# Kernel optimization log

Hardware: AMD Instinct MI355X
Metric: run time of the kernel (lower is better)

The kernel has to match this reference:

```python
import jax, jax.numpy as jnp
import numpy as np
import math

B, S, D, H, L, DFF = 64, 512, 512, 8, 2, 1024
DK = D // H
NEG = -1e32
LN_EPS = 1e-5


def cosine_pos_emb(seqlen, d_model):
    # pe[:,0::2]=sin(pos*div), pe[:,1::2]=cos(pos*div) -- fully overwrites the randn init
    pos = jnp.arange(seqlen, dtype=jnp.float32)[:, None]
    div = jnp.exp(jnp.arange(0, d_model, 2, dtype=jnp.float32) * (-math.log(10000.0) / d_model))
    ang = pos * div  # [S, D/2]
    return jnp.stack([jnp.sin(ang), jnp.cos(ang)], axis=-1).reshape(seqlen, d_model)


def layernorm(x, g, b):
    m = jnp.mean(x, axis=-1, keepdims=True)
    v = jnp.var(x, axis=-1, keepdims=True)
    return g * (x - m) * jax.lax.rsqrt(v + LN_EPS) + b


def setup_inputs() -> dict:
    key = jax.random.key(0)
    ks = jax.random.split(key, 8)
    sc = 0.02
    inp = {
        'q_embed_data': jax.random.normal(ks[0], (B, S, D), jnp.float32),
        'qa_embed_data': jax.random.normal(ks[1], (B, S, D), jnp.float32),
        'forget_rate': jax.random.uniform(ks[2], (B, 1, S, 1), jnp.float32),
        # per-block params, leading dim = n_blocks (kq_same=1: q uses k_linear)
        'Wk': jax.random.normal(ks[3], (L, D, D), jnp.float32) * sc,
        'bk': jnp.zeros((L, D), jnp.float32),
        'Wv': jax.random.normal(ks[4], (L, D, D), jnp.float32) * sc,
        'bv': jnp.zeros((L, D), jnp.float32),
        'Wo': jax.random.normal(ks[5], (L, D, D), jnp.float32) * sc,
        'bo': jnp.zeros((L, D), jnp.float32),
        'ln1_g': jnp.ones((L, D), jnp.float32),
        'ln1_b': jnp.zeros((L, D), jnp.float32),
        'W1': jax.random.normal(ks[6], (L, D, DFF), jnp.float32) * sc,
        'b1': jnp.zeros((L, DFF), jnp.float32),
        'W2': jax.random.normal(ks[7], (L, DFF, D), jnp.float32) * sc,
        'b2': jnp.zeros((L, D), jnp.float32),
        'ln2_g': jnp.ones((L, D), jnp.float32),
        'ln2_b': jnp.zeros((L, D), jnp.float32),
    }
    return inp


def reference(q_embed_data, qa_embed_data, forget_rate, Wk, bk, Wv, bv, Wo, bo,
              ln1_g, ln1_b, W1, b1, W2, b2, ln2_g, ln2_b):
    pe = cosine_pos_emb(S, D)
    x = q_embed_data + pe  # query/key stream
    y = qa_embed_data + pe  # value stream (fixed across blocks)
    # mask=0 path: np.triu(ones, k=0) == 0 -> strictly lower-triangular allowed
    allow = jnp.tril(jnp.ones((S, S), dtype=bool), -1)
    scale = 1.0 / math.sqrt(DK)
    for i in range(L):
        qk = (x @ Wk[i] + bk[i]).reshape(B, S, H, DK).transpose(0, 2, 1, 3)  # [B,H,S,dk]
        v = (y @ Wv[i] + bv[i]).reshape(B, S, H, DK).transpose(0, 2, 1, 3)
        scores = jnp.einsum('bhqd,bhkd->bhqk', qk, qk) * scale
        scores = scores * forget_rate  # [B,1,S,1] broadcasts over heads and keys
        scores = jnp.where(allow, scores, NEG)
        p = jax.nn.softmax(scores, axis=-1)
        p = p.at[:, :, 0, :].set(0.0)  # zero_pad: first query row zeroed
        attn = jnp.einsum('bhqk,bhkd->bhqd', p, v).transpose(0, 2, 1, 3).reshape(B, S, D)
        attn = attn @ Wo[i] + bo[i]
        x = layernorm(x + attn, ln1_g[i], ln1_b[i])
        ff = jax.nn.relu(x @ W1[i] + b1[i]) @ W2[i] + b2[i]
        x = layernorm(x + ff, ln2_g[i], ln2_b[i])
    return x
```

## Files before the change

### kernel.cpp

```cpp
#include <hip/hip_runtime.h>
#include <cstdio>

#define B_   64
#define S_   512
#define D_   512
#define H_   8
#define DK_  64
#define DFF_ 1024
#define L_   2
#define BS_  (B_ * S_)

typedef __attribute__((ext_vector_type(8))) short bf16x8;
typedef __attribute__((ext_vector_type(4))) short bf16x4;
typedef __attribute__((ext_vector_type(4))) float f32x4;

__device__ inline short f2bf(float f) {
  unsigned u = __float_as_uint(f);
  u = u + 0x7FFF + ((u >> 16) & 1);
  return (short)(u >> 16);
}
__device__ inline float bf2f(short s) {
  return __uint_as_float(((unsigned)(unsigned short)s) << 16);
}

__device__ inline void gl_lds16(const short* g, void* lds_base) {
  __builtin_amdgcn_global_load_lds(
      (const __attribute__((address_space(1))) void*)g,
      (__attribute__((address_space(3))) void*)lds_base, 16, 0, 0);
}

__global__ void pe_kernel(float* __restrict__ pe) {
  int idx = blockIdx.x * 256 + threadIdx.x;
  int s = idx >> 9, d = idx & 511;
  float dv = __expf((float)(d & ~1) * (-9.210340371976184f / (float)D_));
  float ang = (float)s * dv;
  pe[idx] = (d & 1) ? cosf(ang) : sinf(ang);
}

__global__ __launch_bounds__(256) void prep_kernel(
    const float* __restrict__ q, const float* __restrict__ qa,
    const float* __restrict__ pe,
    short* __restrict__ xb, short* __restrict__ yb) {
  size_t base = ((size_t)blockIdx.x * 256 + threadIdx.x) * 8;
  int sd = (int)(base & (size_t)(S_ * D_ - 1));
  f32x4 p0 = *(const f32x4*)(pe + sd);
  f32x4 p1 = *(const f32x4*)(pe + sd + 4);
  f32x4 q0 = *(const f32x4*)(q + base);
  f32x4 q1 = *(const f32x4*)(q + base + 4);
  f32x4 a0 = *(const f32x4*)(qa + base);
  f32x4 a1 = *(const f32x4*)(qa + base + 4);
  bf16x8 xv, yv;
#pragma unroll
  for (int i = 0; i < 4; ++i) {
    xv[i] = f2bf(q0[i] + p0[i]);
    yv[i] = f2bf(a0[i] + p0[i]);
  }
#pragma unroll
  for (int i = 0; i < 4; ++i) {
    xv[4 + i] = f2bf(q1[i] + p1[i]);
    yv[4 + i] = f2bf(a1[i] + p1[i]);
  }
  *(bf16x8*)(xb + base) = xv;
  *(bf16x8*)(yb + base) = yv;
}

struct TrArgs {
  const float* src[10];
  short* dst[10];
  int R[10], C[10];
};
__global__ __launch_bounds__(256) void tr_w_all(TrArgs a) {
  const int slot = blockIdx.z;
  const int R = a.R[slot], C = a.C[slot];
  const int c0 = blockIdx.x * 64, r0 = blockIdx.y * 64;
  if (c0 >= C || r0 >= R) return;
  const float* __restrict__ src = a.src[slot];
  short* __restrict__ dst = a.dst[slot];
  __shared__ short Ts[64][72];
  const int t = threadIdx.x;
#pragma unroll
  for (int it = 0; it < 2; ++it) {
    int c2 = it * 256 + t;
    int srow = c2 >> 3, schunk = c2 & 7;
    const float* sp = src + (size_t)(r0 + srow) * C + c0 + schunk * 8;
    f32x4 a0 = *(const f32x4*)sp;
    f32x4 a1 = *(const f32x4*)(sp + 4);
#pragma unroll
    for (int k = 0; k < 4; ++k) Ts[srow][schunk * 8 + k] = f2bf(a0[k]);
#pragma unroll
    for (int k = 0; k < 4; ++k) Ts[srow][schunk * 8 + 4 + k] = f2bf(a1[k]);
  }
  __syncthreads();
#pragma unroll
  for (int it = 0; it < 2; ++it) {
    int c2 = it * 256 + t;
    int orow = c2 >> 3, ochunk = c2 & 7;
    bf16x8 vv;
#pragma unroll
    for (int k = 0; k < 8; ++k) vv[k] = Ts[ochunk * 8 + k][orow];
    *(bf16x8*)(dst + (size_t)(c0 + orow) * R + r0 + ochunk * 8) = vv;
  }
}

__global__ __launch_bounds__(256, 2) void gemm_bt(
    const short* __restrict__ A, const short* __restrict__ BT,
    const float* __restrict__ bias, short* __restrict__ Cb,
    int M, int N, int K, int relu, int bias_row, int nx, int xmaj)
{
  const int nwg = gridDim.x;
  const int cpx = nwg >> 3;
  const int l = (blockIdx.x & 7) * cpx + (blockIdx.x >> 3);
  int bcol, brow;
  if (xmaj) { bcol = l % nx; brow = l / nx; }
  else      { int ny = nwg / nx; brow = l % ny; bcol = l / ny; }

  __shared__ __align__(16) short As[2][128][32];
  __shared__ __align__(16) short Bs[2][256][32];
  const int t = threadIdx.x;
  const int w = t >> 6, lane = t & 63, lr = lane & 15, lk = lane >> 4;
  const int wr = w >> 1, wc = w & 1;

  const f32x4 vzero = {0.f, 0.f, 0.f, 0.f};
  f32x4 acc[4][8];
#pragma unroll
  for (int m = 0; m < 4; ++m)
#pragma unroll
    for (int n = 0; n < 8; ++n) acc[m][n] = vzero;

  const short* Abase = A + (size_t)brow * 128 * K;
  const short* Bbase = BT + (size_t)bcol * 256 * K;

  auto stage = [&](int buf, int k0) {
#pragma unroll
    for (int it = 0; it < 2; ++it) {
      int cb = it * 256 + w * 64;
      int c = cb + lane;
      gl_lds16(Abase + (size_t)(c >> 2) * K + k0 + (c & 3) * 8, (char*)&As[buf][0][0] + (size_t)cb * 16);
    }
#pragma unroll
    for (int it = 0; it < 4; ++it) {
      int cb = it * 256 + w * 64;
      int c = cb + lane;
      gl_lds16(Bbase + (size_t)(c >> 2) * K + k0 + (c & 3) * 8, (char*)&Bs[buf][0][0] + (size_t)cb * 16);
    }
  };

  stage(0, 0);
  int cur = 0;
  for (int k0 = 0; k0 < K; k0 += 32) {
    if (k0 + 32 < K) {
      stage(cur ^ 1, k0 + 32);
      asm volatile("s_waitcnt vmcnt(6)" ::: "memory");
    } else {
      asm volatile("s_waitcnt vmcnt(0)" ::: "memory");
    }
    asm volatile("s_barrier" ::: "memory");

    bf16x8 af[4], bf[8];
#pragma unroll
    for (int m = 0; m < 4; ++m) af[m] = *(const bf16x8*)&As[cur][wr * 64 + m * 16 + lr][lk * 8];
#pragma unroll
    for (int n = 0; n < 8; ++n) bf[n] = *(const bf16x8*)&Bs[cur][wc * 128 + n * 16 + lr][lk * 8];
#pragma unroll
    for (int m = 0; m < 4; ++m)
#pragma unroll
      for (int n = 0; n < 8; ++n)
        acc[m][n] = __builtin_amdgcn_mfma_f32_16x16x32_bf16(bf[n], af[m], acc[m][n], 0, 0, 0);

    asm volatile("s_barrier" ::: "memory");
    cur ^= 1;
  }

#pragma unroll
  for (int m = 0; m < 4; ++m) {
    int row = brow * 128 + wr * 64 + m * 16 + lr;
    float brv = (bias && bias_row) ? bias[row] : 0.f;
    size_t rb = (size_t)row * N;
#pragma unroll
    for (int n = 0; n < 8; ++n) {
      int colb = bcol * 256 + wc * 128 + n * 16 + lk * 4;
      f32x4 bv4;
      if (bias && !bias_row) bv4 = *(const f32x4*)(bias + colb);
      else { bv4[0] = brv; bv4[1] = brv; bv4[2] = brv; bv4[3] = brv; }
      bf16x4 ov;
#pragma unroll
      for (int j = 0; j < 4; ++j) {
        float vv = acc[m][n][j] + bv4[j];
        if (relu) vv = fmaxf(vv, 0.f);
        ov[j] = f2bf(vv);
      }
      *(bf16x4*)(Cb + rb + colb) = ov;
    }
  }
}

template<int P>
__device__ __forceinline__ void attn_body(
    const short* __restrict__ qk, const short* __restrict__ vT,
    const float* __restrict__ fr, short* __restrict__ out,
    short (*Pl)[552], float (*redsum)[32][4],
    int h, int b, int w, int lr, int lk)
{
  constexpr int qo0 = 32 * P, qo1 = 32 * (15 - P);
  constexpr int c0 = 2 * P + 2;
  constexpr int colb1 = c0 * 16;
  constexpr int n0 = P + 1;
  constexpr int n1 = 16 - P;

  const size_t qk_head = (size_t)b * S_ * D_ + (size_t)h * DK_;
  const float scale = 0.125f;

  bf16x8 qf0[2][2], qf1[2][2];
#pragma unroll
  for (int qt = 0; qt < 2; ++qt)
#pragma unroll
    for (int ks = 0; ks < 2; ++ks) {
      qf0[qt][ks] = *(const bf16x8*)(qk + qk_head + (size_t)(qo0 + qt * 16 + lr) * D_ + ks * 32 + lk * 8);
      qf1[qt][ks] = *(const bf16x8*)(qk + qk_head + (size_t)(qo1 + qt * 16 + lr) * D_ + ks * 32 + lk * 8);
    }

  float frv0[2], frv1[2];
#pragma unroll
  for (int qt = 0; qt < 2; ++qt) {
    frv0[qt] = scale * fr[(size_t)b * S_ + qo0 + qt * 16 + lr];
    frv1[qt] = scale * fr[(size_t)b * S_ + qo1 + qt * 16 + lr];
  }

  const f32x4 vzero = {0.f, 0.f, 0.f, 0.f};
  f32x4 acc[9][2];
#pragma unroll
  for (int i = 0; i < 9; ++i) { acc[i][0] = vzero; acc[i][1] = vzero; }

  const int nfr = (w < 2) ? 9 : 8;
  const short* kqbase = qk + qk_head + (size_t)lr * D_ + lk * 8;
  auto kfoff = [&](int i) -> size_t {
    int f = w + 4 * i;
    int kt = (f < c0) ? f : f - c0;
    return (size_t)kt * 16 * D_;
  };
  bf16x8 kreg[4][2];
#pragma unroll
  for (int i = 0; i < 4; ++i) {
    if (i < nfr) {
      const short* p = kqbase + kfoff(i);
      kreg[i][0] = *(const bf16x8*)p;
      kreg[i][1] = *(const bf16x8*)(p + 32);
    }
  }
  __builtin_amdgcn_sched_barrier(0);
#pragma unroll
  for (int i = 0; i < 9; ++i) {
    if (i < nfr) {
      const int f = w + 4 * i;
      __builtin_amdgcn_s_setprio(1);
      if (f < c0) {
#pragma unroll
        for (int ks = 0; ks < 2; ++ks) {
          acc[i][0] = __builtin_amdgcn_mfma_f32_16x16x32_bf16(kreg[i & 3][ks], qf0[0][ks], acc[i][0], 0, 0, 0);
          acc[i][1] = __builtin_amdgcn_mfma_f32_16x16x32_bf16(kreg[i & 3][ks], qf0[1][ks], acc[i][1], 0, 0, 0);
        }
      } else {
#pragma unroll
        for (int ks = 0; ks < 2; ++ks) {
          acc[i][0] = __builtin_amdgcn_mfma_f32_16x16x32_bf16(kreg[i & 3][ks], qf1[0][ks], acc[i][0], 0, 0, 0);
          acc[i][1] = __builtin_amdgcn_mfma_f32_16x16x32_bf16(kreg[i & 3][ks], qf1[1][ks], acc[i][1], 0, 0, 0);
        }
      }
      __builtin_amdgcn_s_setprio(0);
      __builtin_amdgcn_sched_barrier(0);
      if (i + 4 < nfr) {
        const short* p = kqbase + kfoff(i + 4);
        kreg[i & 3][0] = *(const bf16x8*)p;
        kreg[i & 3][1] = *(const bf16x8*)(p + 32);
      }
      __builtin_amdgcn_sched_barrier(0);
    }
  }

  const int uqt0 = w & 1, udh0 = w >> 1;
  const int uqt1 = w >> 1, udh1 = w & 1;
  const short* vu0 = vT + (size_t)(h * DK_ + udh0 * 32 + lr) * BS_ + (size_t)b * S_ + lk * 8;
  const short* vu1 = vT + (size_t)(h * DK_ + udh1 * 32 + lr) * BS_ + (size_t)b * S_ + lk * 8;
  bf16x8 vfB[3][2][2];
#pragma unroll
  for (int kb = 0; kb < 3; ++kb) {
    if (kb < n0) {
#pragma unroll
      for (int n = 0; n < 2; ++n)
        vfB[kb][0][n] = *(const bf16x8*)(vu0 + (size_t)n * 16 * BS_ + kb * 32);
    }
    if (kb < n1) {
#pragma unroll
      for (int n = 0; n < 2; ++n)
        vfB[kb][1][n] = *(const bf16x8*)(vu1 + (size_t)n * 16 * BS_ + kb * 32);
    }
  }
  __builtin_amdgcn_sched_barrier(0);

  float rs00 = 0.f, rs01 = 0.f, rs10 = 0.f, rs11 = 0.f;
#pragma unroll
  for (int frag = 0; frag < 34; ++frag) {
    if ((frag & 3) == w) {
      const int i = frag >> 2;
      const int tl = (frag < c0) ? 0 : 1;
      const int kt = tl ? frag - c0 : frag;
      const int kbase = kt * 16 + lk * 4;
      const int colb = (tl ? colb1 : 0) + kbase;
#pragma unroll
      for (int qt = 0; qt < 2; ++qt) {
        int qrow = (tl ? qo1 : qo0) + qt * 16 + lr;
        float fv = tl ? frv1[qt] : frv0[qt];
        bf16x4 pk;
        float rs = 0.f;
#pragma unroll
        for (int j = 0; j < 4; ++j) {
          float e = (kbase + j < qrow) ? __expf(acc[i][qt][j] * fv) : 0.f;
          rs += e;
          pk[j] = f2bf(e);
        }
        *(bf16x4*)&Pl[qt * 16 + lr][colb] = pk;
        if (tl == 0) { if (qt == 0) rs00 += rs; else rs01 += rs; }
        else         { if (qt == 0) rs10 += rs; else rs11 += rs; }
      }
    }
  }

#pragma unroll
  for (int msk = 16; msk < 64; msk <<= 1) {
    rs00 += __shfl_xor(rs00, msk);
    rs01 += __shfl_xor(rs01, msk);
    rs10 += __shfl_xor(rs10, msk);
    rs11 += __shfl_xor(rs11, msk);
  }
  if (lk == 0) {
    redsum[0][lr][w] = rs00;
    redsum[0][16 + lr][w] = rs01;
    redsum[1][lr][w] = rs10;
    redsum[1][16 + lr][w] = rs11;
  }
  __syncthreads();

  const short* prow0 = &Pl[uqt0 * 16 + lr][lk * 8];
  const short* prow1 = &Pl[uqt1 * 16 + lr][colb1 + lk * 8];
  f32x4 oacc0[2] = {vzero, vzero}, oacc1[2] = {vzero, vzero};
  bf16x8 paB[2][2];
  paB[0][0] = *(const bf16x8*)prow0;
  paB[0][1] = *(const bf16x8*)prow1;

#pragma unroll
  for (int kb = 0; kb < 16; ++kb) {
    const int sc = kb % 3;
    const int pc = kb & 1, pn = pc ^ 1;
    if (kb + 1 < n0) paB[pn][0] = *(const bf16x8*)(prow0 + (kb + 1) * 32);
    if (kb + 1 < n1) paB[pn][1] = *(const bf16x8*)(prow1 + (kb + 1) * 32);
    __builtin_amdgcn_sched_barrier(0);
    __builtin_amdgcn_s_setprio(1);
    if (kb < n0) {
#pragma unroll
      for (int n = 0; n < 2; ++n)
        oacc0[n] = __builtin_amdgcn_mfma_f32_16x16x32_bf16(paB[pc][0], vfB[sc][0][n], oacc0[n], 0, 0, 0);
    }
    if (kb < n1) {
#pragma unroll
      for (int n = 0; n < 2; ++n)
        oacc1[n] = __builtin_amdgcn_mfma_f32_16x16x32_bf16(paB[pc][1], vfB[sc][1][n], oacc1[n], 0, 0, 0);
    }
    __builtin_amdgcn_s_setprio(0);
    __builtin_amdgcn_sched_barrier(0);
    if (kb + 3 < n0) {
#pragma unroll
      for (int n = 0; n < 2; ++n)
        vfB[sc][0][n] = *(const bf16x8*)(vu0 + (size_t)n * 16 * BS_ + (kb + 3) * 32);
    }
    if (kb + 3 < n1) {
#pragma unroll
      for (int n = 0; n < 2; ++n)
        vfB[sc][1][n] = *(const bf16x8*)(vu1 + (size_t)n * 16 * BS_ + (kb + 3) * 32);
    }
    __builtin_amdgcn_sched_barrier(0);
  }

  {
    float invd[4];
#pragma unroll
    for (int j = 0; j < 4; ++j) {
      int row = uqt0 * 16 + lk * 4 + j;
      float ds = redsum[0][row][0] + redsum[0][row][1] + redsum[0][row][2] + redsum[0][row][3];
      invd[j] = ds > 0.f ? 1.f / ds : 0.f;
    }
#pragma unroll
    for (int n = 0; n < 2; ++n)
#pragma unroll
      for (int j = 0; j < 4; ++j) {
        int qrow = qo0 + uqt0 * 16 + lk * 4 + j;
        out[qk_head + (size_t)qrow * D_ + udh0 * 32 + n * 16 + lr] = f2bf(oacc0[n][j] * invd[j]);
      }
  }
  {
    float invd[4];
#pragma unroll
    for (int j = 0; j < 4; ++j) {
      int row = uqt1 * 16 + lk * 4 + j;
      float ds = redsum[1][row][0] + redsum[1][row][1] + redsum[1][row][2] + redsum[1][row][3];
      invd[j] = ds > 0.f ? 1.f / ds : 0.f;
    }
#pragma unroll
    for (int n = 0; n < 2; ++n)
#pragma unroll
      for (int j = 0; j < 4; ++j) {
        int qrow = qo1 + uqt1 * 16 + lk * 4 + j;
        out[qk_head + (size_t)qrow * D_ + udh1 * 32 + n * 16 + lr] = f2bf(oacc1[n][j] * invd[j]);
      }
  }
}

__global__ __launch_bounds__(256, 3) void attn_kernel(
    const short* __restrict__ qk, const short* __restrict__ vT,
    const float* __restrict__ fr, short* __restrict__ out)
{
  const int hw = blockIdx.x;
  const int l = (hw & 7) * 512 + (hw >> 3);
  const int p = l & 7, hb = l >> 3;
  const int h = hb & 7, b = hb >> 3;
  const int t = threadIdx.x;
  const int w = t >> 6, lr = t & 15, lk = (t & 63) >> 4;

  __shared__ short Pl[32][552];
  __shared__ float redsum[2][32][4];

  switch (p) {
    case 0: attn_body<0>(qk, vT, fr, out, Pl, redsum, h, b, w, lr, lk); break;
    case 1: attn_body<1>(qk, vT, fr, out, Pl, redsum, h, b, w, lr, lk); break;
    case 2: attn_body<2>(qk, vT, fr, out, Pl, redsum, h, b, w, lr, lk); break;
    case 3: attn_body<3>(qk, vT, fr, out, Pl, redsum, h, b, w, lr, lk); break;
    case 4: attn_body<4>(qk, vT, fr, out, Pl, redsum, h, b, w, lr, lk); break;
    case 5: attn_body<5>(qk, vT, fr, out, Pl, redsum, h, b, w, lr, lk); break;
    case 6: attn_body<6>(qk, vT, fr, out, Pl, redsum, h, b, w, lr, lk); break;
    case 7: attn_body<7>(qk, vT, fr, out, Pl, redsum, h, b, w, lr, lk); break;
  }
}

template<int FINAL>
__global__ __launch_bounds__(256) void ln_res_t(
    const short* __restrict__ xin, const short* __restrict__ add,
    const float* __restrict__ g, const float* __restrict__ bb,
    short* __restrict__ xbout, float* __restrict__ fout)
{
  const int row = blockIdx.x * 4 + (threadIdx.x >> 6);
  const int lane = threadIdx.x & 63;
  const size_t base = (size_t)row * D_ + lane * 8;

  bf16x8 xv = *(const bf16x8*)(xin + base);
  bf16x8 av = *(const bf16x8*)(add + base);
  float vals[8];
#pragma unroll
  for (int i = 0; i < 8; ++i) vals[i] = bf2f(xv[i]) + bf2f(av[i]);

  float s = 0.f, sq = 0.f;
#pragma unroll
  for (int i = 0; i < 8; ++i) { s += vals[i]; sq += vals[i] * vals[i]; }
#pragma unroll
  for (int m = 1; m < 64; m <<= 1) { s += __shfl_xor(s, m); sq += __shfl_xor(sq, m); }

  float mean = s * (1.f / D_);
  float var = sq * (1.f / D_) - mean * mean;
  float rstd = rsqrtf(var + 1e-5f);

  int col = lane * 8;
  if (FINAL) {
    f32x4 o0, o1;
#pragma unroll
    for (int i = 0; i < 8; ++i) {
      float vv = g[col + i] * (vals[i] - mean) * rstd + bb[col + i];
      if (i < 4) o0[i] = vv; else o1[i - 4] = vv;
    }
    *(f32x4*)(fout + base) = o0;
    *(f32x4*)(fout + base + 4) = o1;
  } else {
    bf16x8 ob;
#pragma unroll
    for (int i = 0; i < 8; ++i)
      ob[i] = f2bf(g[col + i] * (vals[i] - mean) * rstd + bb[col + i]);
    *(bf16x8*)(xbout + base) = ob;
  }
}

extern "C" void kernel_launch(void* const* d_in, const int* in_sizes, int n_in,
                              void* d_out, int out_size, void* d_ws, size_t ws_size,
                              hipStream_t stream) {
  const float* q_emb = (const float*)d_in[0];
  const float* qa_emb = (const float*)d_in[1];
  const float* frate = (const float*)d_in[2];
  const float* Wk = (const float*)d_in[3];
  const float* bk = (const float*)d_in[4];
  const float* Wv = (const float*)d_in[5];
  const float* bv = (const float*)d_in[6];
  const float* Wo = (const float*)d_in[7];
  const float* bo = (const float*)d_in[8];
  const float* ln1g = (const float*)d_in[9];
  const float* ln1b = (const float*)d_in[10];
  const float* W1 = (const float*)d_in[11];
  const float* b1 = (const float*)d_in[12];
  const float* W2 = (const float*)d_in[13];
  const float* b2 = (const float*)d_in[14];
  const float* ln2g = (const float*)d_in[15];
  const float* ln2b = (const float*)d_in[16];
  float* x = (float*)d_out;

  char* ws = (char*)d_ws;
  size_t off = 0;
  auto alloc = [&](size_t bytes) -> void* {
    void* p = ws + off;
    off += (bytes + 255) & ~(size_t)255;
    return p;
  };
  const size_t MTOK = (size_t)BS_;
  float* pe    = (float*)alloc((size_t)S_ * D_ * 4);
  short* xb    = (short*)alloc(MTOK * D_ * 2);
  short* yb    = (short*)alloc(MTOK * D_ * 2);
  short* qkb   = (short*)alloc(MTOK * D_ * 2);
  short* vTb   = (short*)alloc(MTOK * D_ * 2);
  short* ff1b  = (short*)alloc(MTOK * DFF_ * 2);
  short* attnb = ff1b;
  short* goutb = qkb;
  short* wT[L_][5];
  for (int i = 0; i < L_; ++i) {
    wT[i][0] = (short*)alloc((size_t)D_ * D_ * 2);
    wT[i][1] = (short*)alloc((size_t)D_ * D_ * 2);
    wT[i][2] = (short*)alloc((size_t)D_ * D_ * 2);
    wT[i][3] = (short*)alloc((size_t)D_ * DFF_ * 2);
    wT[i][4] = (short*)alloc((size_t)DFF_ * D_ * 2);
  }
  if (off > ws_size) {
    fprintf(stderr, "parKT: workspace overflow: need %zu have %zu\n", off, ws_size);
    return;
  }

  pe_kernel<<<(S_ * D_) / 256, 256, 0, stream>>>(pe);
  prep_kernel<<<(int)(MTOK * D_ / (256 * 8)), 256, 0, stream>>>(q_emb, qa_emb, pe, xb, yb);

  TrArgs ta;
  for (int i = 0; i < L_; ++i) {
    ta.src[i * 5 + 0] = Wk + (size_t)i * D_ * D_;  ta.dst[i * 5 + 0] = wT[i][0]; ta.R[i * 5 + 0] = D_;   ta.C[i * 5 + 0] = D_;
    ta.src[i * 5 + 1] = Wv + (size_t)i * D_ * D_;  ta.dst[i * 5 + 1] = wT[i][1]; ta.R[i * 5 + 1] = D_;   ta.C[i * 5 + 1] = D_;
    ta.src[i * 5 + 2] = Wo + (size_t)i * D_ * D_;  ta.dst[i * 5 + 2] = wT[i][2]; ta.R[i * 5 + 2] = D_;   ta.C[i * 5 + 2] = D_;
    ta.src[i * 5 + 3] = W1 + (size_t)i * D_ * DFF_; ta.dst[i * 5 + 3] = wT[i][3]; ta.R[i * 5 + 3] = D_;   ta.C[i * 5 + 3] = DFF_;
    ta.src[i * 5 + 4] = W2 + (size_t)i * DFF_ * D_; ta.dst[i * 5 + 4] = wT[i][4]; ta.R[i * 5 + 4] = DFF_; ta.C[i * 5 + 4] = D_;
  }
  tr_w_all<<<dim3(DFF_ / 64, DFF_ / 64, 10), 256, 0, stream>>>(ta);

  const int M = (int)MTOK;
  for (int i = 0; i < L_; ++i) {
    gemm_bt<<<(M / 128) * (D_ / 256), 256, 0, stream>>>(xb, wT[i][0], bk + (size_t)i * D_, qkb, M, D_, D_, 0, 0, D_ / 256, 1);
    gemm_bt<<<(D_ / 128) * (M / 256), 256, 0, stream>>>(wT[i][1], yb, bv + (size_t)i * D_, vTb, D_, M, D_, 0, 1, M / 256, 0);
    attn_kernel<<<(S_ / 64) * H_ * B_, 256, 0, stream>>>(qkb, vTb, frate, attnb);
    gemm_bt<<<(M / 128) * (D_ / 256), 256, 0, stream>>>(attnb, wT[i][2], bo + (size_t)i * D_, goutb, M, D_, D_, 0, 0, D_ / 256, 1);
    ln_res_t<0><<<M / 4, 256, 0, stream>>>(xb, goutb, ln1g + (size_t)i * D_, ln1b + (size_t)i * D_, xb, nullptr);
    gemm_bt<<<(M / 128) * (DFF_ / 256), 256, 0, stream>>>(xb, wT[i][3], b1 + (size_t)i * DFF_, ff1b, M, DFF_, D_, 1, 0, DFF_ / 256, 1);
    gemm_bt<<<(M / 128) * (D_ / 256), 256, 0, stream>>>(ff1b, wT[i][4], b2 + (size_t)i * D_, goutb, M, D_, DFF_, 0, 0, D_ / 256, 1);
    if (i == L_ - 1)
      ln_res_t<1><<<M / 4, 256, 0, stream>>>(xb, goutb, ln2g + (size_t)i * D_, ln2b + (size_t)i * D_, nullptr, x);
    else
      ln_res_t<0><<<M / 4, 256, 0, stream>>>(xb, goutb, ln2g + (size_t)i * D_, ln2b + (size_t)i * D_, xb, nullptr);
  }
}
```

Before: 723.9 us.

## Triple-buffer GEMM LDS tiles with single barrier and XOR-swizzled segments

The bf16 GEMM moves from a double to a triple LDS buffer. Each k-step now needs one barrier instead of two, and the tile two steps ahead is staged after the barrier. Global-to-LDS loads permute the 16-byte segments within each row by an XOR of row bits, and fragment reads apply the matching swizzle to reduce LDS bank conflicts. The cost is higher LDS use per block, up to 72KB, which may reduce occupancy below the two blocks the launch bounds target. The attention kernel only gains alignment attributes.

```diff
diff --git a/kernel.cpp b/kernel.cpp
--- a/kernel.cpp
+++ b/kernel.cpp
@@ -114,11 +114,12 @@
   if (xmaj) { bcol = l % nx; brow = l / nx; }
   else      { int ny = nwg / nx; brow = l % ny; bcol = l / ny; }
 
-  __shared__ __align__(16) short As[2][128][32];
-  __shared__ __align__(16) short Bs[2][256][32];
+  __shared__ __align__(16) short As[3][128][32];
+  __shared__ __align__(16) short Bs[3][256][32];
   const int t = threadIdx.x;
   const int w = t >> 6, lane = t & 63, lr = lane & 15, lk = lane >> 4;
   const int wr = w >> 1, wc = w & 1;
+  const int sw = (lr >> 1) & 3;
 
   const f32x4 vzero = {0.f, 0.f, 0.f, 0.f};
   f32x4 acc[4][8];
@@ -135,40 +136,47 @@
     for (int it = 0; it < 2; ++it) {
       int cb = it * 256 + w * 64;
       int c = cb + lane;
-      gl_lds16(Abase + (size_t)(c >> 2) * K + k0 + (c & 3) * 8, (char*)&As[buf][0][0] + (size_t)cb * 16);
+      int row = c >> 2, seg = c & 3;
+      int segg = seg ^ ((row >> 1) & 3);
+      gl_lds16(Abase + (size_t)row * K + k0 + segg * 8, (char*)&As[buf][0][0] + (size_t)cb * 16);
     }
 #pragma unroll
     for (int it = 0; it < 4; ++it) {
       int cb = it * 256 + w * 64;
       int c = cb + lane;
-      gl_lds16(Bbase + (size_t)(c >> 2) * K + k0 + (c & 3) * 8, (char*)&Bs[buf][0][0] + (size_t)cb * 16);
+      int row = c >> 2, seg = c & 3;
+      int segg = seg ^ ((row >> 1) & 3);
+      gl_lds16(Bbase + (size_t)row * K + k0 + segg * 8, (char*)&Bs[buf][0][0] + (size_t)cb * 16);
     }
   };
 
+  const int ntiles = K >> 5;
   stage(0, 0);
-  int cur = 0;
-  for (int k0 = 0; k0 < K; k0 += 32) {
-    if (k0 + 32 < K) {
-      stage(cur ^ 1, k0 + 32);
+  if (ntiles > 1) stage(1, 32);
+  int cur = 0, nxt = 2;
+  for (int ti = 0; ti < ntiles; ++ti) {
+    if (ti + 1 < ntiles) {
       asm volatile("s_waitcnt vmcnt(6)" ::: "memory");
     } else {
       asm volatile("s_waitcnt vmcnt(0)" ::: "memory");
     }
     asm volatile("s_barrier" ::: "memory");
 
+    if (ti + 2 < ntiles) stage(nxt, (ti + 2) * 32);
+
     bf16x8 af[4], bf[8];
 #pragma unroll
-    for (int m = 0; m < 4; ++m) af[m] = *(const bf16x8*)&As[cur][wr * 64 + m * 16 + lr][lk * 8];
-#pragma unroll
-    for (int n = 0; n < 8; ++n) bf[n] = *(const bf16x8*)&Bs[cur][wc * 128 + n * 16 + lr][lk * 8];
+    for (int m = 0; m < 4; ++m) af[m] = *(const bf16x8*)&As[cur][wr * 64 + m * 16 + lr][(lk ^ sw) * 8];
+#pragma unroll
+    for (int n = 0; n < 8; ++n) bf[n] = *(const bf16x8*)&Bs[cur][wc * 128 + n * 16 + lr][(lk ^ sw) * 8];
 #pragma unroll
     for (int m = 0; m < 4; ++m)
 #pragma unroll
       for (int n = 0; n < 8; ++n)
         acc[m][n] = __builtin_amdgcn_mfma_f32_16x16x32_bf16(bf[n], af[m], acc[m][n], 0, 0, 0);
 
-    asm volatile("s_barrier" ::: "memory");
-    cur ^= 1;
+    cur = (cur == 2) ? 0 : cur + 1;
+    nxt = (nxt == 2) ? 0 : nxt + 1;
   }
 
 #pragma unroll
@@ -349,8 +357,7 @@
 
 #pragma unroll
   for (int kb = 0; kb < 16; ++kb) {
-    const int sc = kb % 3;
-    const int pc = kb & 1, pn = pc ^ 1;
+    const int sc = kb % 3, pc = kb & 1, pn = pc ^ 1;
     if (kb + 1 < n0) paB[pn][0] = *(const bf16x8*)(prow0 + (kb + 1) * 32);
     if (kb + 1 < n1) paB[pn][1] = *(const bf16x8*)(prow1 + (kb + 1) * 32);
     __builtin_amdgcn_sched_barrier(0);
@@ -425,8 +432,8 @@
   const int t = threadIdx.x;
   const int w = t >> 6, lr = t & 15, lk = (t & 63) >> 4;
 
-  __shared__ short Pl[32][552];
-  __shared__ float redsum[2][32][4];
+  __shared__ __align__(16) short Pl[32][552];
+  __shared__ __align__(16) float redsum[2][32][4];
 
   switch (p) {
     case 0: attn_body<0>(qk, vT, fr, out, Pl, redsum, h, b, w, lr, lk); break;
```

After: 727.9 us. About the same (+0.5%).

## Rework GEMM to 256x256 tiles with 512 threads, K=64 steps and XOR-swizzled LDS

Applied to the files above, without the earlier changes.

Rewrites the bf16 GEMM kernel to use 256x256 output tiles with 8 waves of 512 threads, each wave owning a 128x64 sub-tile. The K step grows from 32 to 64. LDS rows are XOR-swizzled per 16-byte chunk to avoid bank conflicts on fragment reads. The goal is more data reuse per loaded byte and fewer global loads per MFMA. In exchange, the grid has half as many workgroups, LDS use per block is 128 KB, and the kernel now waits for all loads (vmcnt(0)) and adds a barrier inside each of the four sub-steps per K tile, which could limit overlap and occupancy.

```diff
diff --git a/kernel.cpp b/kernel.cpp
--- a/kernel.cpp
+++ b/kernel.cpp
@@ -102,7 +102,7 @@
   }
 }
 
-__global__ __launch_bounds__(256, 2) void gemm_bt(
+__global__ __launch_bounds__(512, 2) void gemm_bt(
     const short* __restrict__ A, const short* __restrict__ BT,
     const float* __restrict__ bias, short* __restrict__ Cb,
     int M, int N, int K, int relu, int bias_row, int nx, int xmaj)
@@ -114,71 +114,96 @@
   if (xmaj) { bcol = l % nx; brow = l / nx; }
   else      { int ny = nwg / nx; brow = l % ny; bcol = l / ny; }
 
-  __shared__ __align__(16) short As[2][128][32];
-  __shared__ __align__(16) short Bs[2][256][32];
+  __shared__ __align__(16) short As[2][256 * 64];
+  __shared__ __align__(16) short Bs[2][256 * 64];
   const int t = threadIdx.x;
   const int w = t >> 6, lane = t & 63, lr = lane & 15, lk = lane >> 4;
-  const int wr = w >> 1, wc = w & 1;
+  const int wm = w >> 2, wn = w & 3;
 
   const f32x4 vzero = {0.f, 0.f, 0.f, 0.f};
-  f32x4 acc[4][8];
-#pragma unroll
-  for (int m = 0; m < 4; ++m)
-#pragma unroll
-    for (int n = 0; n < 8; ++n) acc[m][n] = vzero;
-
-  const short* Abase = A + (size_t)brow * 128 * K;
+  f32x4 acc[8][4];
+#pragma unroll
+  for (int m = 0; m < 8; ++m)
+#pragma unroll
+    for (int n = 0; n < 4; ++n) acc[m][n] = vzero;
+
+  const short* Abase = A + (size_t)brow * 256 * K;
   const short* Bbase = BT + (size_t)bcol * 256 * K;
 
-  auto stage = [&](int buf, int k0) {
+  auto stageH = [&](short* lds, const short* gsrc, int half, int k0) {
 #pragma unroll
     for (int it = 0; it < 2; ++it) {
-      int cb = it * 256 + w * 64;
-      int c = cb + lane;
-      gl_lds16(Abase + (size_t)(c >> 2) * K + k0 + (c & 3) * 8, (char*)&As[buf][0][0] + (size_t)cb * 16);
-    }
-#pragma unroll
-    for (int it = 0; it < 4; ++it) {
-      int cb = it * 256 + w * 64;
-      int c = cb + lane;
-      gl_lds16(Bbase + (size_t)(c >> 2) * K + k0 + (c & 3) * 8, (char*)&Bs[buf][0][0] + (size_t)cb * 16);
+      int c = it * 512 + t;
+      int cb = it * 512 + w * 64;
+      int row = half * 128 + (c >> 3);
+      int seg = (c & 7) ^ (row & 7);
+      gl_lds16(gsrc + (size_t)row * K + k0 + seg * 8,
+               (char*)lds + (size_t)(half * 1024 + cb) * 16);
     }
   };
-
-  stage(0, 0);
-  int cur = 0;
-  for (int k0 = 0; k0 < K; k0 += 32) {
-    if (k0 + 32 < K) {
-      stage(cur ^ 1, k0 + 32);
-      asm volatile("s_waitcnt vmcnt(6)" ::: "memory");
-    } else {
-      asm volatile("s_waitcnt vmcnt(0)" ::: "memory");
-    }
+  auto ldfrag = [&](const short* lds, int row, int s) -> bf16x8 {
+    int chunk = row * 8 + (s ^ (row & 7));
+    return *(const bf16x8*)((const char*)lds + (size_t)chunk * 16);
+  };
+
+  const int T = K >> 6;
+  stageH(&As[0][0], Abase, 0, 0);
+  stageH(&As[0][0], Abase, 1, 0);
+  stageH(&Bs[0][0], Bbase, 0, 0);
+  stageH(&Bs[0][0], Bbase, 1, 0);
+
+  for (int ti = 0; ti < T; ++ti) {
+    const int cbuf = ti & 1, obuf = cbuf ^ 1;
+    asm volatile("s_waitcnt vmcnt(0)" ::: "memory");
     asm volatile("s_barrier" ::: "memory");
 
-    bf16x8 af[4], bf[8];
-#pragma unroll
-    for (int m = 0; m < 4; ++m) af[m] = *(const bf16x8*)&As[cur][wr * 64 + m * 16 + lr][lk * 8];
-#pragma unroll
-    for (int n = 0; n < 8; ++n) bf[n] = *(const bf16x8*)&Bs[cur][wc * 128 + n * 16 + lr][lk * 8];
-#pragma unroll
-    for (int m = 0; m < 4; ++m)
-#pragma unroll
-      for (int n = 0; n < 8; ++n)
-        acc[m][n] = __builtin_amdgcn_mfma_f32_16x16x32_bf16(bf[n], af[m], acc[m][n], 0, 0, 0);
-
-    asm volatile("s_barrier" ::: "memory");
-    cur ^= 1;
-  }
-
-#pragma unroll
-  for (int m = 0; m < 4; ++m) {
-    int row = brow * 128 + wr * 64 + m * 16 + lr;
+    if (ti + 1 < T) {
+      int k1 = (ti + 1) * 64;
+      stageH(&As[obuf][0], Abase, 0, k1);
+      stageH(&As[obuf][0], Abase, 1, k1);
+      stageH(&Bs[obuf][0], Bbase, 0, k1);
+      stageH(&Bs[obuf][0], Bbase, 1, k1);
+    }
+
+    bf16x8 bf[4][2];
+#pragma unroll
+    for (int n = 0; n < 4; ++n)
+#pragma unroll
+      for (int kk = 0; kk < 2; ++kk)
+        bf[n][kk] = ldfrag(&Bs[cbuf][0], wn * 64 + n * 16 + lr, kk * 4 + lk);
+
+#pragma unroll
+    for (int p = 0; p < 4; ++p) {
+      bf16x8 af[2][2];
+#pragma unroll
+      for (int mm = 0; mm < 2; ++mm)
+#pragma unroll
+        for (int kk = 0; kk < 2; ++kk)
+          af[mm][kk] = ldfrag(&As[cbuf][0], wm * 128 + (p * 2 + mm) * 16 + lr, kk * 4 + lk);
+      __builtin_amdgcn_sched_barrier(0);
+      __builtin_amdgcn_s_setprio(1);
+#pragma unroll
+      for (int mm = 0; mm < 2; ++mm)
+#pragma unroll
+        for (int n = 0; n < 4; ++n)
+#pragma unroll
+          for (int kk = 0; kk < 2; ++kk)
+            acc[p * 2 + mm][n] = __builtin_amdgcn_mfma_f32_16x16x32_bf16(
+                bf[n][kk], af[mm][kk], acc[p * 2 + mm][n], 0, 0, 0);
+      __builtin_amdgcn_s_setprio(0);
+      __builtin_amdgcn_sched_barrier(0);
+      asm volatile("s_barrier" ::: "memory");
+    }
+  }
+
+#pragma unroll
+  for (int m = 0; m < 8; ++m) {
+    int row = brow * 256 + wm * 128 + m * 16 + lr;
     float brv = (bias && bias_row) ? bias[row] : 0.f;
     size_t rb = (size_t)row * N;
 #pragma unroll
-    for (int n = 0; n < 8; ++n) {
-      int colb = bcol * 256 + wc * 128 + n * 16 + lk * 4;
+    for (int n = 0; n < 4; ++n) {
+      int colb = bcol * 256 + wn * 64 + n * 16 + lk * 4;
       f32x4 bv4;
       if (bias && !bias_row) bv4 = *(const f32x4*)(bias + colb);
       else { bv4[0] = brv; bv4[1] = brv; bv4[2] = brv; bv4[3] = brv; }
@@ -349,8 +374,7 @@
 
 #pragma unroll
   for (int kb = 0; kb < 16; ++kb) {
-    const int sc = kb % 3;
-    const int pc = kb & 1, pn = pc ^ 1;
+    const int sc = kb % 3, pc = kb & 1, pn = pc ^ 1;
     if (kb + 1 < n0) paB[pn][0] = *(const bf16x8*)(prow0 + (kb + 1) * 32);
     if (kb + 1 < n1) paB[pn][1] = *(const bf16x8*)(prow1 + (kb + 1) * 32);
     __builtin_amdgcn_sched_barrier(0);
@@ -425,8 +449,8 @@
   const int t = threadIdx.x;
   const int w = t >> 6, lr = t & 15, lk = (t & 63) >> 4;
 
-  __shared__ short Pl[32][552];
-  __shared__ float redsum[2][32][4];
+  __shared__ __align__(16) short Pl[32][552];
+  __shared__ __align__(16) float redsum[2][32][4];
 
   switch (p) {
     case 0: attn_body<0>(qk, vT, fr, out, Pl, redsum, h, b, w, lr, lk); break;
@@ -551,13 +575,13 @@
 
   const int M = (int)MTOK;
   for (int i = 0; i < L_; ++i) {
-    gemm_bt<<<(M / 128) * (D_ / 256), 256, 0, stream>>>(xb, wT[i][0], bk + (size_t)i * D_, qkb, M, D_, D_, 0, 0, D_ / 256, 1);
-    gemm_bt<<<(D_ / 128) * (M / 256), 256, 0, stream>>>(wT[i][1], yb, bv + (size_t)i * D_, vTb, D_, M, D_, 0, 1, M / 256, 0);
+    gemm_bt<<<(M / 256) * (D_ / 256), 512, 0, stream>>>(xb, wT[i][0], bk + (size_t)i * D_, qkb, M, D_, D_, 0, 0, D_ / 256, 1);
+    gemm_bt<<<(D_ / 256) * (M / 256), 512, 0, stream>>>(wT[i][1], yb, bv + (size_t)i * D_, vTb, D_, M, D_, 0, 1, M / 256, 0);
     attn_kernel<<<(S_ / 64) * H_ * B_, 256, 0, stream>>>(qkb, vTb, frate, attnb);
-    gemm_bt<<<(M / 128) * (D_ / 256), 256, 0, stream>>>(attnb, wT[i][2], bo + (size_t)i * D_, goutb, M, D_, D_, 0, 0, D_ / 256, 1);
+    gemm_bt<<<(M / 256) * (D_ / 256), 512, 0, stream>>>(attnb, wT[i][2], bo + (size_t)i * D_, goutb, M, D_, D_, 0, 0, D_ / 256, 1);
     ln_res_t<0><<<M / 4, 256, 0, stream>>>(xb, goutb, ln1g + (size_t)i * D_, ln1b + (size_t)i * D_, xb, nullptr);
-    gemm_bt<<<(M / 128) * (DFF_ / 256), 256, 0, stream>>>(xb, wT[i][3], b1 + (size_t)i * DFF_, ff1b, M, DFF_, D_, 1, 0, DFF_ / 256, 1);
-    gemm_bt<<<(M / 128) * (D_ / 256), 256, 0, stream>>>(ff1b, wT[i][4], b2 + (size_t)i * D_, goutb, M, D_, DFF_, 0, 0, D_ / 256, 1);
+    gemm_bt<<<(M / 256) * (DFF_ / 256), 512, 0, stream>>>(xb, wT[i][3], b1 + (size_t)i * DFF_, ff1b, M, DFF_, D_, 1, 0, DFF_ / 256, 1);
+    gemm_bt<<<(M / 256) * (D_ / 256), 512, 0, stream>>>(ff1b, wT[i][4], b2 + (size_t)i * D_, goutb, M, D_, DFF_, 0, 0, D_ / 256, 1);
     if (i == L_ - 1)
       ln_res_t<1><<<M / 4, 256, 0, stream>>>(xb, goutb, ln2g + (size_t)i * D_, ln2b + (size_t)i * D_, nullptr, x);
     else
```

Result: no change. 735.0 us (+1.5%).
